# Optimization experiments

Hardware: AMD Instinct MI355X
Metric: run time of the kernel (lower is better)

The kernel has to match this reference:

```python
import jax, jax.numpy as jnp
import numpy as np

B, T, C, H, S = 4, 2048, 1024, 16, 64
LN_EPS = 1e-5
WKV_EPS = 1e-6
K_CLAMP = 30.0


def _ln(x, g, b):
    m = jnp.mean(x, axis=-1, keepdims=True)
    v = jnp.var(x, axis=-1, keepdims=True)
    return (x - m) * jax.lax.rsqrt(v + LN_EPS) * g + b


def _wkv(k, v, time_decay, time_first):
    # k, v: [B,T,H,S]; recurrence in fp32 over time
    decay = jnp.exp(-jnp.exp(time_decay.astype(jnp.float32)))  # [H,S]
    tf = jnp.exp(time_first.astype(jnp.float32))               # [H,S]
    kt = jnp.moveaxis(k, 1, 0).astype(jnp.float32)  # [T,B,H,S]
    vt = jnp.moveaxis(v, 1, 0).astype(jnp.float32)
    # t == 0 special case: state seeded with time_first factor
    w0 = jnp.exp(jnp.minimum(kt[0], K_CLAMP))
    num0 = tf * w0 * vt[0]
    den0 = tf * w0

    def step(carry, xs):
        num, den = carry
        kk, vv = xs
        w = jnp.exp(jnp.minimum(kk, K_CLAMP))
        num = decay * num + w * vv
        den = decay * den + w
        return (num, den), num / (den + WKV_EPS)

    (_, _), rest = jax.lax.scan(step, (num0, den0), (kt[1:], vt[1:]))
    out = jnp.concatenate([(num0 / (den0 + WKV_EPS))[None], rest], axis=0)  # [T,B,H,S]
    return jnp.moveaxis(out, 0, 1)  # [B,T,H,S]


def setup_inputs() -> dict:
    key = jax.random.key(0)
    ks = jax.random.split(key, 8)
    sc = 1.0 / np.sqrt(C)
    sc4 = 1.0 / np.sqrt(4 * C)
    return {
        "x": jax.random.normal(ks[0], (B, T, C), jnp.float32),
        "time_decay": jnp.full((H, S), -5.0, jnp.float32),
        "time_first": jnp.zeros((H, S), jnp.float32),
        "Wk": jax.random.normal(ks[1], (C, C), jnp.float32) * sc,
        "Wv": jax.random.normal(ks[2], (C, C), jnp.float32) * sc,
        "Wr": jax.random.normal(ks[3], (C, C), jnp.float32) * sc,
        "Wo": jax.random.normal(ks[4], (C, C), jnp.float32) * sc,
        "Wffk": jax.random.normal(ks[5], (4 * C, C), jnp.float32) * sc,
        "Wffv": jax.random.normal(ks[6], (C, 4 * C), jnp.float32) * sc4,
        "ln1_g": jnp.ones((C,), jnp.float32),
        "ln1_b": jnp.zeros((C,), jnp.float32),
        "ln2_g": jnp.ones((C,), jnp.float32),
        "ln2_b": jnp.zeros((C,), jnp.float32),
    }


def reference(x, time_decay, time_first, Wk, Wv, Wr, Wo, Wffk, Wffv, ln1_g, ln1_b, ln2_g, ln2_b):
    b, t, c = x.shape
    h, s = time_decay.shape
    xl = _ln(x, ln1_g, ln1_b)
    k = (xl @ Wk.T).reshape(b, t, h, s)
    v = (xl @ Wv.T).reshape(b, t, h, s)
    r = (xl @ Wr.T).reshape(b, t, h, s)
    wkv = _wkv(k, v, time_decay, time_first).astype(x.dtype)
    rwkv = (jax.nn.sigmoid(r) * wkv).reshape(b, t, c)
    x = x + rwkv @ Wo.T
    xl2 = _ln(x, ln2_g, ln2_b)
    ffn = (jax.nn.relu(xl2 @ Wffk.T) ** 2) @ Wffv.T
    return x + ffn
```

## Files before the change

kernel.cpp:

```cpp
#include <hip/hip_runtime.h>
#include <cstdint>
#include <cstddef>

#define TT 2048
#define CC 1024
#define HH 16
#define SS 64
#define MROWS 8192
#define KVRN 3072
#define NCH 32
#define LCH 64

using short8 = __attribute__((ext_vector_type(8))) short;
using f32x4  = __attribute__((ext_vector_type(4))) float;

__device__ __forceinline__ float b2f(unsigned short u) {
  union { unsigned int i; float f; } c; c.i = ((unsigned int)u) << 16; return c.f;
}
__device__ __forceinline__ unsigned short f2b(float f) {
  union { float f; unsigned int i; } c; c.f = f;
  unsigned int r = c.i + 0x7fffu + ((c.i >> 16) & 1u);
  return (unsigned short)(r >> 16);
}

typedef const __attribute__((address_space(1))) unsigned int* gas_ptr;
typedef __attribute__((address_space(3))) unsigned int* las_ptr;
__device__ __forceinline__ void gl_lds16(const unsigned short* g, unsigned short* l) {
  __builtin_amdgcn_global_load_lds((gas_ptr)g, (las_ptr)l, 16, 0, 0);
}

__global__ __launch_bounds__(256) void cvt_all(const float* __restrict__ Wk,
                                               const float* __restrict__ Wv,
                                               const float* __restrict__ Wr,
                                               const float* __restrict__ Wo,
                                               const float* __restrict__ Wffk,
                                               const float* __restrict__ Wffv,
                                               unsigned short* __restrict__ dst) {
  const size_t M1 = 1048576;
  size_t i = ((size_t)blockIdx.x * 256 + threadIdx.x) * 4;
  const float* src; size_t off;
  if      (i <  1 * M1) { src = Wk;   off = 0;      }
  else if (i <  2 * M1) { src = Wv;   off = 1 * M1; }
  else if (i <  3 * M1) { src = Wr;   off = 2 * M1; }
  else if (i <  4 * M1) { src = Wo;   off = 3 * M1; }
  else if (i <  8 * M1) { src = Wffk; off = 4 * M1; }
  else                  { src = Wffv; off = 8 * M1; }
  float4 v = *(const float4*)(src + (i - off));
  *(ushort4*)(dst + i) = make_ushort4(f2b(v.x), f2b(v.y), f2b(v.z), f2b(v.w));
}

__global__ __launch_bounds__(256) void ln_kernel(const float* __restrict__ x,
                                                 const float* __restrict__ g,
                                                 const float* __restrict__ bta,
                                                 unsigned short* __restrict__ out) {
  const int row = blockIdx.x;
  const int tid = threadIdx.x;
  const float* xr = x + (size_t)row * CC;
  float4 v = *(const float4*)(xr + tid * 4);
  float s  = v.x + v.y + v.z + v.w;
  float ss = v.x * v.x + v.y * v.y + v.z * v.z + v.w * v.w;
#pragma unroll
  for (int off = 32; off > 0; off >>= 1) {
    s  += __shfl_xor(s, off, 64);
    ss += __shfl_xor(ss, off, 64);
  }
  __shared__ float ls[4], lss[4];
  if ((tid & 63) == 0) { ls[tid >> 6] = s; lss[tid >> 6] = ss; }
  __syncthreads();
  s  = ls[0] + ls[1] + ls[2] + ls[3];
  ss = lss[0] + lss[1] + lss[2] + lss[3];
  const float mean = s * (1.0f / CC);
  const float var  = ss * (1.0f / CC) - mean * mean;
  const float rstd = rsqrtf(var + 1e-5f);
  float4 gv = *(const float4*)(g + tid * 4);
  float4 bv = *(const float4*)(bta + tid * 4);
  ushort4 o = make_ushort4(f2b((v.x - mean) * rstd * gv.x + bv.x),
                           f2b((v.y - mean) * rstd * gv.y + bv.y),
                           f2b((v.z - mean) * rstd * gv.z + bv.z),
                           f2b((v.w - mean) * rstd * gv.w + bv.w));
  *(ushort4*)(out + (size_t)row * CC + tid * 4) = o;
}

__global__ __launch_bounds__(64) void wkv_local(const unsigned short* __restrict__ kvr,
                                                const float* __restrict__ td,
                                                const float* __restrict__ tfp,
                                                float* __restrict__ scratch) {
  const int blk = blockIdx.x;
  const int bh = blk >> 5, c = blk & (NCH - 1);
  const int b = bh >> 4, h = bh & 15;
  const int s = threadIdx.x;
  const int ch = h * SS + s;
  const float e = __expf(td[ch]);
  const float d = __expf(-e);
  const float tfir = __expf(tfp[ch]);
  size_t idx = ((size_t)b * TT + (size_t)c * LCH) * KVRN + ch;
  float num = 0.f, den = 0.f;
  for (int i = 0; i < LCH; ++i) {
    float w = __expf(fminf(b2f(kvr[idx]), 30.f));
    if (c == 0 && i == 0) w *= tfir;
    float vv = b2f(kvr[idx + 1024]);
    num = d * num + w * vv;
    den = d * den + w;
    idx += KVRN;
  }
  float* o = scratch + ((size_t)bh * NCH + c) * 128;
  o[s] = num; o[64 + s] = den;
}

__global__ __launch_bounds__(64) void wkv_emit(const unsigned short* __restrict__ kvr,
                                               const float* __restrict__ td,
                                               const float* __restrict__ tfp,
                                               const float* __restrict__ scratch,
                                               unsigned short* __restrict__ rwkv) {
  const int blk = blockIdx.x;
  const int bh = blk >> 5, c = blk & (NCH - 1);
  const int b = bh >> 4, h = bh & 15;
  const int s = threadIdx.x;
  const int ch = h * SS + s;
  const float e = __expf(td[ch]);
  const float d = __expf(-e);
  const float Dc = __expf(-e * (float)LCH);
  const float tfir = __expf(tfp[ch]);
  float num = 0.f, den = 0.f;
  const float* sc = scratch + (size_t)bh * NCH * 128;
  for (int cc = 0; cc < c; ++cc) {
    num = Dc * num + sc[cc * 128 + s];
    den = Dc * den + sc[cc * 128 + 64 + s];
  }
  size_t idx = ((size_t)b * TT + (size_t)c * LCH) * KVRN + ch;
  size_t odx = ((size_t)b * TT + (size_t)c * LCH) * CC + ch;
  for (int i = 0; i < LCH; ++i) {
    float w = __expf(fminf(b2f(kvr[idx]), 30.f));
    if (c == 0 && i == 0) w *= tfir;
    float vv = b2f(kvr[idx + 1024]);
    num = d * num + w * vv;
    den = d * den + w;
    float o = num / (den + 1e-6f);
    float rr = b2f(kvr[idx + 2048]);
    float sg = 1.0f / (1.0f + __expf(-rr));
    rwkv[odx] = f2b(sg * o);
    idx += KVRN;
    odx += CC;
  }
}

template <int EP>
__global__ __launch_bounds__(256, 4) void gemm_bt(const unsigned short* __restrict__ A,
                                                  const unsigned short* __restrict__ Bw,
                                                  void* __restrict__ outv,
                                                  const float* __restrict__ res,
                                                  int N, int K) {
  __shared__ __align__(16) unsigned short As[2][128 * 32];
  __shared__ __align__(16) unsigned short Bs[2][128 * 32];
  const int tid = threadIdx.x;

  const int nbn = N >> 7;
  const int per_grp = nbn << 4;
  const int bid = blockIdx.x;
  const int grp = bid / per_grp;
  const int rem = bid - grp * per_grp;
  const int bm = (grp << 4) + (rem & 15);
  const int bn = rem >> 4;

  const int ch0 = tid, ch1 = tid + 256;
  const int r0 = ch0 >> 2, q0 = (ch0 & 3) ^ ((ch0 >> 3) & 3);
  const int r1 = ch1 >> 2, q1 = (ch1 & 3) ^ ((ch1 >> 3) & 3);
  const unsigned short* ga0 = A  + (size_t)(bm * 128 + r0) * K + q0 * 8;
  const unsigned short* ga1 = A  + (size_t)(bm * 128 + r1) * K + q1 * 8;
  const unsigned short* gb0 = Bw + (size_t)(bn * 128 + r0) * K + q0 * 8;
  const unsigned short* gb1 = Bw + (size_t)(bn * 128 + r1) * K + q1 * 8;
  const int so0 = ch0 * 8, so1 = ch1 * 8;

  const int lane = tid & 63;
  const int w    = tid >> 6;
  const int q    = lane >> 4, r16 = lane & 15;
  const int qs   = q ^ ((r16 >> 1) & 3);
  const int wrow = (w >> 1) * 64, wcol = (w & 1) * 64;

  f32x4 acc[4][4] = {};

  gl_lds16(ga0, &As[0][so0]);
  gl_lds16(ga1, &As[0][so1]);
  gl_lds16(gb0, &Bs[0][so0]);
  gl_lds16(gb1, &Bs[0][so1]);
  ga0 += 32; ga1 += 32; gb0 += 32; gb1 += 32;

  int buf = 0;
  for (int k0 = 0; k0 < K; k0 += 32) {
    __syncthreads();
    if (k0 + 32 < K) {
      const int nb = buf ^ 1;
      gl_lds16(ga0, &As[nb][so0]);
      gl_lds16(ga1, &As[nb][so1]);
      gl_lds16(gb0, &Bs[nb][so0]);
      gl_lds16(gb1, &Bs[nb][so1]);
      ga0 += 32; ga1 += 32; gb0 += 32; gb1 += 32;
    }
    const unsigned short* Ab = &As[buf][0];
    const unsigned short* Bb = &Bs[buf][0];
    short8 af[4], bfr[4];
#pragma unroll
    for (int mi = 0; mi < 4; ++mi)
      af[mi] = *(const short8*)(Ab + ((wrow + mi * 16 + r16) * 4 + qs) * 8);
#pragma unroll
    for (int ni = 0; ni < 4; ++ni)
      bfr[ni] = *(const short8*)(Bb + ((wcol + ni * 16 + r16) * 4 + qs) * 8);
#pragma unroll
    for (int mi = 0; mi < 4; ++mi)
#pragma unroll
      for (int ni = 0; ni < 4; ++ni)
        acc[mi][ni] = __builtin_amdgcn_mfma_f32_16x16x32_bf16(af[mi], bfr[ni], acc[mi][ni], 0, 0, 0);
    buf ^= 1;
  }

#pragma unroll
  for (int mi = 0; mi < 4; ++mi) {
#pragma unroll
    for (int r = 0; r < 4; ++r) {
      const int grow = bm * 128 + wrow + mi * 16 + q * 4 + r;
#pragma unroll
      for (int ni = 0; ni < 4; ++ni) {
        const int gcol = bn * 128 + wcol + ni * 16 + r16;
        const size_t idx = (size_t)grow * N + gcol;
        float vv = acc[mi][ni][r];
        if (EP == 2) {
          ((float*)outv)[idx] = res[idx] + vv;
        } else {
          if (EP == 1) { vv = fmaxf(vv, 0.0f); vv = vv * vv; }
          ((unsigned short*)outv)[idx] = f2b(vv);
        }
      }
    }
  }
}

extern "C" void kernel_launch(void* const* d_in, const int* in_sizes, int n_in,
                              void* d_out, int out_size, void* d_ws, size_t ws_size,
                              hipStream_t stream) {
  const float* x    = (const float*)d_in[0];
  const float* td   = (const float*)d_in[1];
  const float* tf   = (const float*)d_in[2];
  const float* Wk   = (const float*)d_in[3];
  const float* Wv   = (const float*)d_in[4];
  const float* Wr   = (const float*)d_in[5];
  const float* Wo   = (const float*)d_in[6];
  const float* Wffk = (const float*)d_in[7];
  const float* Wffv = (const float*)d_in[8];
  const float* g1   = (const float*)d_in[9];
  const float* b1   = (const float*)d_in[10];
  const float* g2   = (const float*)d_in[11];
  const float* b2   = (const float*)d_in[12];
  float* out = (float*)d_out;

  char* ws = (char*)d_ws;
  const size_t MB = 1024ull * 1024ull;
  unsigned short* WB    = (unsigned short*)ws;
  unsigned short* WkvrB = WB;
  unsigned short* WoB   = WB + 3 * 1048576;
  unsigned short* WfkB  = WB + 4 * 1048576;
  unsigned short* WfvB  = WB + 8 * 1048576;
  unsigned short* xl    = (unsigned short*)(ws + 24 * MB);
  unsigned short* kvr   = (unsigned short*)(ws + 40 * MB);
  float*          x2    = (float*)(ws + 88 * MB);
  unsigned short* hb    = (unsigned short*)(ws + 120 * MB);
  float*          wkvS  = (float*)(ws + 184 * MB);
  unsigned short* rwkv  = xl;
  unsigned short* xl2   = kvr;

  cvt_all<<<12288, 256, 0, stream>>>(Wk, Wv, Wr, Wo, Wffk, Wffv, WB);

  ln_kernel<<<MROWS, 256, 0, stream>>>(x, g1, b1, xl);

  gemm_bt<0><<<(KVRN / 128) * (MROWS / 128), 256, 0, stream>>>(xl, WkvrB, kvr, nullptr, KVRN, 1024);

  wkv_local<<<64 * NCH, 64, 0, stream>>>(kvr, td, tf, wkvS);
  wkv_emit<<<64 * NCH, 64, 0, stream>>>(kvr, td, tf, wkvS, rwkv);

  gemm_bt<2><<<(CC / 128) * (MROWS / 128), 256, 0, stream>>>(rwkv, WoB, x2, x, 1024, 1024);

  ln_kernel<<<MROWS, 256, 0, stream>>>(x2, g2, b2, xl2);

  gemm_bt<1><<<(4096 / 128) * (MROWS / 128), 256, 0, stream>>>(xl2, WfkB, hb, nullptr, 4096, 1024);

  gemm_bt<2><<<(CC / 128) * (MROWS / 128), 256, 0, stream>>>(hb, WfvB, out, x2, 1024, 4096);
}
```

Before: 460.5 us.

## Triple-buffer GEMM LDS pipeline and fuse weight conversion with first LayerNorm

The GEMM mainloop moves from two LDS buffers to three, so global-to-LDS loads run two k-steps ahead. A sched_barrier keeps the prefetch issue ahead of the MFMA work, and occupancy drops from 4 to 3 blocks per CU because LDS per block grows. Separately, the weight fp32-to-bf16 conversion and the first LayerNorm are merged into a single launch with disjoint block ranges, saving one kernel launch and letting the two independent jobs overlap. The risks are lower occupancy and whether a single barrier per iteration is enough to protect buffer reuse.

```diff
diff --git a/kernel.cpp b/kernel.cpp
--- a/kernel.cpp
+++ b/kernel.cpp
@@ -29,24 +29,57 @@
   __builtin_amdgcn_global_load_lds((gas_ptr)g, (las_ptr)l, 16, 0, 0);
 }
 
-__global__ __launch_bounds__(256) void cvt_all(const float* __restrict__ Wk,
-                                               const float* __restrict__ Wv,
-                                               const float* __restrict__ Wr,
-                                               const float* __restrict__ Wo,
-                                               const float* __restrict__ Wffk,
-                                               const float* __restrict__ Wffv,
-                                               unsigned short* __restrict__ dst) {
+__global__ __launch_bounds__(256) void cvt_ln_kernel(const float* __restrict__ Wk,
+                                                     const float* __restrict__ Wv,
+                                                     const float* __restrict__ Wr,
+                                                     const float* __restrict__ Wo,
+                                                     const float* __restrict__ Wffk,
+                                                     const float* __restrict__ Wffv,
+                                                     unsigned short* __restrict__ dst,
+                                                     const float* __restrict__ x,
+                                                     const float* __restrict__ g,
+                                                     const float* __restrict__ bta,
+                                                     unsigned short* __restrict__ xlo) {
   const size_t M1 = 1048576;
-  size_t i = ((size_t)blockIdx.x * 256 + threadIdx.x) * 4;
-  const float* src; size_t off;
-  if      (i <  1 * M1) { src = Wk;   off = 0;      }
-  else if (i <  2 * M1) { src = Wv;   off = 1 * M1; }
-  else if (i <  3 * M1) { src = Wr;   off = 2 * M1; }
-  else if (i <  4 * M1) { src = Wo;   off = 3 * M1; }
-  else if (i <  8 * M1) { src = Wffk; off = 4 * M1; }
-  else                  { src = Wffv; off = 8 * M1; }
-  float4 v = *(const float4*)(src + (i - off));
-  *(ushort4*)(dst + i) = make_ushort4(f2b(v.x), f2b(v.y), f2b(v.z), f2b(v.w));
+  const int tid = threadIdx.x;
+  if (blockIdx.x < 12288) {
+    size_t i = ((size_t)blockIdx.x * 256 + tid) * 4;
+    const float* src; size_t off;
+    if      (i <  1 * M1) { src = Wk;   off = 0;      }
+    else if (i <  2 * M1) { src = Wv;   off = 1 * M1; }
+    else if (i <  3 * M1) { src = Wr;   off = 2 * M1; }
+    else if (i <  4 * M1) { src = Wo;   off = 3 * M1; }
+    else if (i <  8 * M1) { src = Wffk; off = 4 * M1; }
+    else                  { src = Wffv; off = 8 * M1; }
+    float4 v = *(const float4*)(src + (i - off));
+    *(ushort4*)(dst + i) = make_ushort4(f2b(v.x), f2b(v.y), f2b(v.z), f2b(v.w));
+    return;
+  }
+  const int row = blockIdx.x - 12288;
+  const float* xr = x + (size_t)row * CC;
+  float4 v = *(const float4*)(xr + tid * 4);
+  float s  = v.x + v.y + v.z + v.w;
+  float ss = v.x * v.x + v.y * v.y + v.z * v.z + v.w * v.w;
+#pragma unroll
+  for (int off = 32; off > 0; off >>= 1) {
+    s  += __shfl_xor(s, off, 64);
+    ss += __shfl_xor(ss, off, 64);
+  }
+  __shared__ float ls[4], lss[4];
+  if ((tid & 63) == 0) { ls[tid >> 6] = s; lss[tid >> 6] = ss; }
+  __syncthreads();
+  s  = ls[0] + ls[1] + ls[2] + ls[3];
+  ss = lss[0] + lss[1] + lss[2] + lss[3];
+  const float mean = s * (1.0f / CC);
+  const float var  = ss * (1.0f / CC) - mean * mean;
+  const float rstd = rsqrtf(var + 1e-5f);
+  float4 gv = *(const float4*)(g + tid * 4);
+  float4 bv = *(const float4*)(bta + tid * 4);
+  ushort4 o = make_ushort4(f2b((v.x - mean) * rstd * gv.x + bv.x),
+                           f2b((v.y - mean) * rstd * gv.y + bv.y),
+                           f2b((v.z - mean) * rstd * gv.z + bv.z),
+                           f2b((v.w - mean) * rstd * gv.w + bv.w));
+  *(ushort4*)(xlo + (size_t)row * CC + tid * 4) = o;
 }
 
 __global__ __launch_bounds__(256) void ln_kernel(const float* __restrict__ x,
@@ -145,13 +178,13 @@
 }
 
 template <int EP>
-__global__ __launch_bounds__(256, 4) void gemm_bt(const unsigned short* __restrict__ A,
+__global__ __launch_bounds__(256, 3) void gemm_bt(const unsigned short* __restrict__ A,
                                                   const unsigned short* __restrict__ Bw,
                                                   void* __restrict__ outv,
                                                   const float* __restrict__ res,
                                                   int N, int K) {
-  __shared__ __align__(16) unsigned short As[2][128 * 32];
-  __shared__ __align__(16) unsigned short Bs[2][128 * 32];
+  __shared__ __align__(16) unsigned short As[3][128 * 32];
+  __shared__ __align__(16) unsigned short Bs[3][128 * 32];
   const int tid = threadIdx.x;
 
   const int nbn = N >> 7;
@@ -179,25 +212,26 @@
 
   f32x4 acc[4][4] = {};
 
-  gl_lds16(ga0, &As[0][so0]);
-  gl_lds16(ga1, &As[0][so1]);
-  gl_lds16(gb0, &Bs[0][so0]);
-  gl_lds16(gb1, &Bs[0][so1]);
-  ga0 += 32; ga1 += 32; gb0 += 32; gb1 += 32;
-
-  int buf = 0;
-  for (int k0 = 0; k0 < K; k0 += 32) {
+  auto stage = [&](int b3) {
+    gl_lds16(ga0, &As[b3][so0]);
+    gl_lds16(ga1, &As[b3][so1]);
+    gl_lds16(gb0, &Bs[b3][so0]);
+    gl_lds16(gb1, &Bs[b3][so1]);
+    ga0 += 32; ga1 += 32; gb0 += 32; gb1 += 32;
+  };
+
+  const int iters = K >> 5;
+  stage(0);
+  stage(1);
+
+  int cb = 0, pb = 2;
+  for (int i = 0; i < iters; ++i) {
     __syncthreads();
-    if (k0 + 32 < K) {
-      const int nb = buf ^ 1;
-      gl_lds16(ga0, &As[nb][so0]);
-      gl_lds16(ga1, &As[nb][so1]);
-      gl_lds16(gb0, &Bs[nb][so0]);
-      gl_lds16(gb1, &Bs[nb][so1]);
-      ga0 += 32; ga1 += 32; gb0 += 32; gb1 += 32;
-    }
-    const unsigned short* Ab = &As[buf][0];
-    const unsigned short* Bb = &Bs[buf][0];
+    if (i + 2 < iters) stage(pb);
+    __builtin_amdgcn_sched_barrier(0);
+
+    const unsigned short* Ab = &As[cb][0];
+    const unsigned short* Bb = &Bs[cb][0];
     short8 af[4], bfr[4];
 #pragma unroll
     for (int mi = 0; mi < 4; ++mi)
@@ -210,7 +244,9 @@
 #pragma unroll
       for (int ni = 0; ni < 4; ++ni)
         acc[mi][ni] = __builtin_amdgcn_mfma_f32_16x16x32_bf16(af[mi], bfr[ni], acc[mi][ni], 0, 0, 0);
-    buf ^= 1;
+
+    cb = (cb == 2) ? 0 : cb + 1;
+    pb = (pb == 2) ? 0 : pb + 1;
   }
 
 #pragma unroll
@@ -267,9 +303,8 @@
   unsigned short* rwkv  = xl;
   unsigned short* xl2   = kvr;
 
-  cvt_all<<<12288, 256, 0, stream>>>(Wk, Wv, Wr, Wo, Wffk, Wffv, WB);
-
-  ln_kernel<<<MROWS, 256, 0, stream>>>(x, g1, b1, xl);
+  cvt_ln_kernel<<<12288 + MROWS, 256, 0, stream>>>(Wk, Wv, Wr, Wo, Wffk, Wffv, WB,
+                                                   x, g1, b1, xl);
 
   gemm_bt<0><<<(KVRN / 128) * (MROWS / 128), 256, 0, stream>>>(xl, WkvrB, kvr, nullptr, KVRN, 1024);
 
```

Result: faster. 444.4 us (-3.5%).
